# Kernel tuning notes

Hardware: AMD Instinct MI355X
Metric: run time of the kernel (lower is better)

## Reference

```python
import jax, jax.numpy as jnp
import numpy as np
import math

PS = 16            # patch size for SigmaPredictor
HID = 8            # hidden_dim
SCALE = HID ** -0.5
SIGMA_CAP = 6.0    # BoundedSoftplus threshold
EPS_S = 1e-6       # BoundedSoftplus eps


def setup_inputs() -> dict:
    key = jax.random.key(0)
    ks = jax.random.split(key, 10)
    B, C, H, W = 2, 1, 384, 384
    d_in = C * PS * PS  # 256
    r = lambda k_, sh: jax.random.normal(k_, sh, dtype=jnp.float32) * 0.1
    z = lambda sh: jnp.zeros(sh, dtype=jnp.float32)
    return {
        "x": jax.random.uniform(ks[0], (B, C, H, W), dtype=jnp.float32),
        "Wq": r(ks[1], (d_in, HID)), "bq": z((HID,)),
        "Wk": r(ks[2], (d_in, HID)), "bk": z((HID,)),
        "Wv": r(ks[3], (d_in, HID)), "bv": z((HID,)),
        "Wsq": r(ks[4], (HID, HID)), "bsq": z((HID,)),
        "Wsk": r(ks[5], (HID, HID)), "bsk": z((HID,)),
        "Wsv": r(ks[6], (HID, HID)), "bsv": z((HID,)),
        "ln_g": jnp.ones((HID,), jnp.float32), "ln_b": z((HID,)),
        "Wp": r(ks[7], (HID, 3)),
        # bias ~4 -> sigmas ~4 -> kernel size k=13 (production-scale support)
        "bp": jnp.full((3,), 4.0, dtype=jnp.float32),
    }


def _attn(q, k, v):
    a = jax.nn.softmax(jnp.einsum('bnd,bmd->bnm', q, k) * SCALE, axis=-1)
    return jnp.einsum('bnm,bmd->bnd', a, v)


def _predict_sigmas(x, Wq, bq, Wk, bk, Wv, bv, Wsq, bsq, Wsk, bsk, Wsv, bsv, ln_g, ln_b, Wp, bp):
    b, c, h, w = x.shape
    Hp, Wn = h // PS, w // PS
    # unfold into non-overlapping patches: [B, Hp*Wn, C*PS*PS]
    pat = x.reshape(b, c, Hp, PS, Wn, PS).transpose(0, 2, 4, 1, 3, 5).reshape(b, Hp * Wn, c * PS * PS)
    feats = _attn(pat @ Wq + bq, pat @ Wk + bk, pat @ Wv + bv)
    o = _attn(feats @ Wsq + bsq, feats @ Wsk + bsk, feats @ Wsv + bsv)
    mu = o.mean(-1, keepdims=True)
    var = ((o - mu) ** 2).mean(-1, keepdims=True)
    o = (o - mu) / jnp.sqrt(var + 1e-5) * ln_g + ln_b
    s = jnp.minimum(jax.nn.softplus(o @ Wp + bp), SIGMA_CAP) + EPS_S  # BoundedSoftplus
    s = s.reshape(b, Hp, Wn, 3)
    # nearest-neighbor upsample to full resolution: [B, H, W, 3]
    return jnp.repeat(jnp.repeat(s, PS, axis=1), PS, axis=2)


def _bilateral(x, s, k):
    b, c, h, w = x.shape
    sx, sy, sr = s[..., 0], s[..., 1], s[..., 2]
    half = k // 2
    xp = jnp.pad(x, ((0, 0), (0, 0), (half, half), (half, half)))
    # [B, C, H, W, k*k], dy-major to match torch unfold/meshgrid ordering
    patches = jnp.stack([xp[:, :, dy:dy + h, dx:dx + w]
                         for dy in range(k) for dx in range(k)], axis=-1)
    coords = jnp.arange(-half, half + 1, dtype=jnp.float32)
    yy, xx = jnp.meshgrid(coords, coords, indexing='ij')
    xx2 = (xx ** 2).reshape(-1)
    yy2 = (yy ** 2).reshape(-1)
    # spatial kernel [B, H, W, k*k]
    sp = jnp.exp(-xx2 / (2 * sx[..., None] ** 2) - yy2 / (2 * sy[..., None] ** 2))
    # range kernel (C == 1 branch) [B, C, H, W, k*k]
    rg = jnp.exp(-(x[..., None] - patches) ** 2 / (2 * sr[:, None, :, :, None] ** 2))
    comb = sp[:, None] * rg
    norm = comb / (comb.sum(-1, keepdims=True) + 1e-8)
    return (patches * norm).sum(-1)


def reference(x, Wq, bq, Wk, bk, Wv, bv, Wsq, bsq, Wsk, bsk, Wsv, bsv, ln_g, ln_b, Wp, bp):
    s = _predict_sigmas(x, Wq, bq, Wk, bk, Wv, bv, Wsq, bsq, Wsk, bsk, Wsv, bsv, ln_g, ln_b, Wp, bp)
    # data-dependent kernel size, computed eagerly (matches torch .item())
    m = float(jnp.maximum(s[..., 0].max(), s[..., 1].max()))
    k = int(2 * math.ceil(m + 1))
    if k % 2 == 0:
        k += 1
    return _bilateral(x, s, k)
```

## Files before the change

### kernel.cpp

```cpp
#include <hip/hip_runtime.h>

#define N_TOK 576
#define HP    24
#define PS    16
#define IMG   384
#define ATTN_SCALE 0.35355339059327373f

__global__ __launch_bounds__(256) void k_qkv1(
    const float* __restrict__ x,
    const float* __restrict__ Wq, const float* __restrict__ bq,
    const float* __restrict__ Wk, const float* __restrict__ bk,
    const float* __restrict__ Wv, const float* __restrict__ bv,
    float* __restrict__ q1, float* __restrict__ k1, float* __restrict__ v1,
    int* __restrict__ smax)
{
    const int lane = threadIdx.x & 63, wv = threadIdx.x >> 6;
    const int idx = blockIdx.x*4 + wv;
    const int b = idx / N_TOK, n = idx % N_TOK;
    const int py = n / HP, px = n % HP;

    if (idx == 0 && lane == 0) atomicExch(smax, 0);

    const int iy = lane >> 2, ix0 = (lane & 3) * 4;
    const float4 pv = *(const float4*)
        &x[b*IMG*IMG + (py*PS + iy)*IMG + px*PS + ix0];

    float acc[24];
#pragma unroll
    for (int j = 0; j < 24; ++j) acc[j] = 0.f;

#pragma unroll
    for (int j = 0; j < 4; ++j) {
        const int t = 4*lane + j;
        const float p = ((const float*)&pv)[j];
#pragma unroll
        for (int h = 0; h < 8; ++h) {
            acc[h]      += p * Wq[t*8 + h];
            acc[8 + h]  += p * Wk[t*8 + h];
            acc[16 + h] += p * Wv[t*8 + h];
        }
    }
#pragma unroll
    for (int off = 32; off; off >>= 1)
#pragma unroll
        for (int j = 0; j < 24; ++j) acc[j] += __shfl_xor(acc[j], off);

    if (lane == 0) {
#pragma unroll
        for (int h = 0; h < 8; ++h) {
            q1[idx*8 + h] = acc[h]      + bq[h];
            k1[idx*8 + h] = acc[8 + h]  + bk[h];
            v1[idx*8 + h] = acc[16 + h] + bv[h];
        }
    }
}

__global__ __launch_bounds__(256) void k_attn1(
    const float* __restrict__ q1, const float* __restrict__ k1, const float* __restrict__ v1,
    const float* __restrict__ Wsq, const float* __restrict__ bsq,
    const float* __restrict__ Wsk, const float* __restrict__ bsk,
    const float* __restrict__ Wsv, const float* __restrict__ bsv,
    float* __restrict__ q2, float* __restrict__ k2, float* __restrict__ v2)
{
    const int lane = threadIdx.x & 63;
    const int wv   = threadIdx.x >> 6;
    const int tok  = blockIdx.x*4 + wv;
    const int b    = tok / N_TOK;

    const float4 qa = *(const float4*)&q1[tok*8];
    const float4 qb = *(const float4*)&q1[tok*8 + 4];

    const float* kbp = k1 + b*N_TOK*8;
    const float* vbp = v1 + b*N_TOK*8;

    float sc[9], mx = -1e30f;
#pragma unroll
    for (int ch = 0; ch < 9; ++ch) {
        const float4* kp = (const float4*)(kbp + (ch*64 + lane)*8);
        const float4 k0 = kp[0], k1v = kp[1];
        float d = qa.x*k0.x + qa.y*k0.y + qa.z*k0.z + qa.w*k0.w
                + qb.x*k1v.x + qb.y*k1v.y + qb.z*k1v.z + qb.w*k1v.w;
        d *= ATTN_SCALE;
        sc[ch] = d;
        mx = fmaxf(mx, d);
    }
#pragma unroll
    for (int off = 32; off; off >>= 1) mx = fmaxf(mx, __shfl_xor(mx, off));

    float ssum = 0.f, o[8];
#pragma unroll
    for (int h = 0; h < 8; ++h) o[h] = 0.f;
#pragma unroll
    for (int ch = 0; ch < 9; ++ch) {
        const float p = __expf(sc[ch] - mx);
        ssum += p;
        const float4* vp = (const float4*)(vbp + (ch*64 + lane)*8);
        const float4 v0 = vp[0], v1v = vp[1];
        o[0] += p*v0.x; o[1] += p*v0.y; o[2] += p*v0.z; o[3] += p*v0.w;
        o[4] += p*v1v.x; o[5] += p*v1v.y; o[6] += p*v1v.z; o[7] += p*v1v.w;
    }
#pragma unroll
    for (int off = 32; off; off >>= 1) {
        ssum += __shfl_xor(ssum, off);
#pragma unroll
        for (int h = 0; h < 8; ++h) o[h] += __shfl_xor(o[h], off);
    }
    const float inv = 1.f/ssum;
    float f[8];
#pragma unroll
    for (int h = 0; h < 8; ++h) f[h] = o[h]*inv;

    if (lane < 24) {
        const int mat = lane >> 3, h = lane & 7;
        const float* Wm = (mat==0)?Wsq:(mat==1)?Wsk:Wsv;
        const float* bm = (mat==0)?bsq:(mat==1)?bsk:bsv;
        float s = bm[h];
#pragma unroll
        for (int j = 0; j < 8; ++j) s += f[j]*Wm[j*8 + h];
        float* dst = (mat==0)?q2:(mat==1)?k2:v2;
        dst[tok*8 + h] = s;
    }
}

__global__ __launch_bounds__(256) void k_attn2(
    const float* __restrict__ q2, const float* __restrict__ k2, const float* __restrict__ v2,
    const float* __restrict__ ln_g, const float* __restrict__ ln_b,
    const float* __restrict__ Wp,   const float* __restrict__ bp,
    float* __restrict__ sig, int* __restrict__ smax)
{
    const int lane = threadIdx.x & 63;
    const int wv   = threadIdx.x >> 6;
    const int tok  = blockIdx.x*4 + wv;
    const int b    = tok / N_TOK;

    const float4 qa = *(const float4*)&q2[tok*8];
    const float4 qb = *(const float4*)&q2[tok*8 + 4];

    const float* kbp = k2 + b*N_TOK*8;
    const float* vbp = v2 + b*N_TOK*8;

    float sc[9], mx = -1e30f;
#pragma unroll
    for (int ch = 0; ch < 9; ++ch) {
        const float4* kp = (const float4*)(kbp + (ch*64 + lane)*8);
        const float4 k0 = kp[0], k1v = kp[1];
        float d = qa.x*k0.x + qa.y*k0.y + qa.z*k0.z + qa.w*k0.w
                + qb.x*k1v.x + qb.y*k1v.y + qb.z*k1v.z + qb.w*k1v.w;
        d *= ATTN_SCALE;
        sc[ch] = d;
        mx = fmaxf(mx, d);
    }
#pragma unroll
    for (int off = 32; off; off >>= 1) mx = fmaxf(mx, __shfl_xor(mx, off));

    float ssum = 0.f, o[8];
#pragma unroll
    for (int h = 0; h < 8; ++h) o[h] = 0.f;
#pragma unroll
    for (int ch = 0; ch < 9; ++ch) {
        const float p = __expf(sc[ch] - mx);
        ssum += p;
        const float4* vp = (const float4*)(vbp + (ch*64 + lane)*8);
        const float4 v0 = vp[0], v1v = vp[1];
        o[0] += p*v0.x; o[1] += p*v0.y; o[2] += p*v0.z; o[3] += p*v0.w;
        o[4] += p*v1v.x; o[5] += p*v1v.y; o[6] += p*v1v.z; o[7] += p*v1v.w;
    }
#pragma unroll
    for (int off = 32; off; off >>= 1) {
        ssum += __shfl_xor(ssum, off);
#pragma unroll
        for (int h = 0; h < 8; ++h) o[h] += __shfl_xor(o[h], off);
    }

    if (lane == 0) {
        const float inv = 1.f/ssum;
        float f[8];
        float mu = 0.f;
#pragma unroll
        for (int h = 0; h < 8; ++h) { f[h] = o[h]*inv; mu += f[h]; }
        mu *= 0.125f;
        float var = 0.f;
#pragma unroll
        for (int h = 0; h < 8; ++h) { const float d = f[h]-mu; var += d*d; }
        var *= 0.125f;
        const float rinv = rsqrtf(var + 1e-5f);
        float on[8];
#pragma unroll
        for (int h = 0; h < 8; ++h)
            on[h] = (f[h]-mu)*rinv*ln_g[h] + ln_b[h];
        float sv[3];
#pragma unroll
        for (int c = 0; c < 3; ++c) {
            float z = bp[c];
#pragma unroll
            for (int j = 0; j < 8; ++j) z += on[j]*Wp[j*3 + c];
            const float sp = (z > 20.f) ? z : log1pf(__expf(z));
            sv[c] = fminf(sp, 6.0f) + 1e-6f;
            sig[tok*3 + c] = sv[c];
        }
        atomicMax(smax, __float_as_int(fmaxf(sv[0], sv[1])));
    }
}

__global__ __launch_bounds__(256) void k_bilat(
    const float* __restrict__ x, const float* __restrict__ sig,
    int* __restrict__ smax, float* __restrict__ out)
{
    __shared__ float tile[32*40];
    __shared__ float spt[17*17];
    __shared__ int   s_half;

    const int blk = blockIdx.x;
    const int b  = blk / N_TOK;
    const int n  = blk % N_TOK;
    const int py = n / HP, px = n % HP;
    const int tx = threadIdx.x & 15, ty = threadIdx.x >> 4;

    if (threadIdx.x == 0) {
        const float m = __int_as_float(atomicMax(smax, 0));
        int h = (int)ceilf(m + 1.0f);
        if (h < 1) h = 1;
        if (h > 8) h = 8;
        s_half = h;
    }
    __syncthreads();
    const int half = s_half;
    const int k = 2*half + 1;
    const int tilew = PS + 2*half;

    const float sx = sig[blk*3 + 0];
    const float sy = sig[blk*3 + 1];
    const float sr = sig[blk*3 + 2];

    const float* xb = x + b*IMG*IMG;
    for (int yy = ty; yy < tilew; yy += 16) {
        const int gy = py*PS + yy - half;
        for (int xx = tx; xx < tilew; xx += 16) {
            const int gx = px*PS + xx - half;
            float v = 0.f;
            if ((unsigned)gy < IMG && (unsigned)gx < IMG)
                v = xb[gy*IMG + gx];
            tile[yy*40 + xx] = v;
        }
    }
    {
        const float axc = -0.5f/(sx*sx);
        const float ayc = -0.5f/(sy*sy);
        for (int i = threadIdx.x; i < k*k; i += 256) {
            const int dy = i / k, dx = i - dy*k;
            const float fy = (float)(dy - half), fx = (float)(dx - half);
            spt[i] = __expf(ayc*fy*fy + axc*fx*fx);
        }
    }
    __syncthreads();

    const float c   = tile[(ty+half)*40 + (tx+half)];
    const float ar2 = -0.72134752044448170f/(sr*sr);

    float num = 0.f, den = 0.f;
    for (int dy = 0; dy < k; ++dy) {
        const float* row = &tile[(ty+dy)*40 + tx];
        const float* spr = &spt[dy*k];
        for (int dx = 0; dx < k; ++dx) {
            const float pix = row[dx];
            const float d   = c - pix;
            const float w   = spr[dx] * exp2f(ar2*d*d);
            den += w;
            num += w*pix;
        }
    }
    out[b*IMG*IMG + (py*PS + ty)*IMG + (px*PS + tx)] = num/(den + 1e-8f);
}

extern "C" void kernel_launch(void* const* d_in, const int* in_sizes, int n_in,
                              void* d_out, int out_size, void* d_ws, size_t ws_size,
                              hipStream_t stream)
{
    const float* x    = (const float*)d_in[0];
    const float* Wq   = (const float*)d_in[1];
    const float* bq   = (const float*)d_in[2];
    const float* Wk   = (const float*)d_in[3];
    const float* bk   = (const float*)d_in[4];
    const float* Wv   = (const float*)d_in[5];
    const float* bv   = (const float*)d_in[6];
    const float* Wsq  = (const float*)d_in[7];
    const float* bsq  = (const float*)d_in[8];
    const float* Wsk  = (const float*)d_in[9];
    const float* bsk  = (const float*)d_in[10];
    const float* Wsv  = (const float*)d_in[11];
    const float* bsv  = (const float*)d_in[12];
    const float* ln_g = (const float*)d_in[13];
    const float* ln_b = (const float*)d_in[14];
    const float* Wp   = (const float*)d_in[15];
    const float* bp   = (const float*)d_in[16];

    float* W  = (float*)d_ws;
    float* q1 = W;
    float* k1 = W +  9216;
    float* v1 = W + 18432;
    float* q2 = W + 27648;
    float* k2 = W + 36864;
    float* v2 = W + 46080;
    float* sg = W + 55296;
    int* smax = (int*)(W + 58752);

    k_qkv1<<<2*N_TOK/4, 256, 0, stream>>>(x, Wq, bq, Wk, bk, Wv, bv,
                                          q1, k1, v1, smax);
    k_attn1<<<2*N_TOK/4, 256, 0, stream>>>(q1, k1, v1, Wsq, bsq, Wsk, bsk,
                                           Wsv, bsv, q2, k2, v2);
    k_attn2<<<2*N_TOK/4, 256, 0, stream>>>(q2, k2, v2, ln_g, ln_b, Wp, bp,
                                           sg, smax);
    k_bilat<<<2*N_TOK, 256, 0, stream>>>(x, sg, smax, (float*)d_out);
}
```

Before: 149.6 us.

## Fuse all four stages into one persistent kernel with grid barriers

Replaces the four separate launches (QKV projection, two attention stages, bilateral filter) with one persistent kernel of 576 blocks that sync through atomic-counter grid barriers. Queries stay in registers between stages, and sigmas go through shared memory instead of global buffers. Each block now runs two bilateral patches back to back. This removes launch overhead and intermediate round-trips, but relies on all 576 blocks being co-resident. It also adds a memset and leaves half the waves idle during the attention phases.

```diff
diff --git a/kernel.cpp b/kernel.cpp
--- a/kernel.cpp
+++ b/kernel.cpp
@@ -5,271 +5,278 @@
 #define PS    16
 #define IMG   384
 #define ATTN_SCALE 0.35355339059327373f
-
-__global__ __launch_bounds__(256) void k_qkv1(
+#define NBLK  576
+
+__device__ __forceinline__ void gbar(unsigned* cnt, unsigned* flag)
+{
+    __syncthreads();
+    if (threadIdx.x == 0) {
+        __threadfence();
+        const unsigned old = __hip_atomic_fetch_add(
+            cnt, 1u, __ATOMIC_ACQ_REL, __HIP_MEMORY_SCOPE_AGENT);
+        if (old == NBLK - 1u) {
+            __hip_atomic_store(flag, 1u, __ATOMIC_RELEASE,
+                               __HIP_MEMORY_SCOPE_AGENT);
+        } else {
+            while (!__hip_atomic_load(flag, __ATOMIC_RELAXED,
+                                      __HIP_MEMORY_SCOPE_AGENT))
+                __builtin_amdgcn_s_sleep(4);
+        }
+        __threadfence();
+    }
+    __syncthreads();
+}
+
+__global__ __launch_bounds__(256, 3) void k_all(
     const float* __restrict__ x,
     const float* __restrict__ Wq, const float* __restrict__ bq,
     const float* __restrict__ Wk, const float* __restrict__ bk,
     const float* __restrict__ Wv, const float* __restrict__ bv,
-    float* __restrict__ q1, float* __restrict__ k1, float* __restrict__ v1,
-    int* __restrict__ smax)
-{
-    const int lane = threadIdx.x & 63, wv = threadIdx.x >> 6;
-    const int idx = blockIdx.x*4 + wv;
-    const int b = idx / N_TOK, n = idx % N_TOK;
-    const int py = n / HP, px = n % HP;
-
-    if (idx == 0 && lane == 0) atomicExch(smax, 0);
-
-    const int iy = lane >> 2, ix0 = (lane & 3) * 4;
-    const float4 pv = *(const float4*)
-        &x[b*IMG*IMG + (py*PS + iy)*IMG + px*PS + ix0];
-
-    float acc[24];
-#pragma unroll
-    for (int j = 0; j < 24; ++j) acc[j] = 0.f;
-
-#pragma unroll
-    for (int j = 0; j < 4; ++j) {
-        const int t = 4*lane + j;
-        const float p = ((const float*)&pv)[j];
-#pragma unroll
-        for (int h = 0; h < 8; ++h) {
-            acc[h]      += p * Wq[t*8 + h];
-            acc[8 + h]  += p * Wk[t*8 + h];
-            acc[16 + h] += p * Wv[t*8 + h];
-        }
-    }
-#pragma unroll
-    for (int off = 32; off; off >>= 1)
-#pragma unroll
-        for (int j = 0; j < 24; ++j) acc[j] += __shfl_xor(acc[j], off);
-
-    if (lane == 0) {
-#pragma unroll
-        for (int h = 0; h < 8; ++h) {
-            q1[idx*8 + h] = acc[h]      + bq[h];
-            k1[idx*8 + h] = acc[8 + h]  + bk[h];
-            v1[idx*8 + h] = acc[16 + h] + bv[h];
-        }
-    }
-}
-
-__global__ __launch_bounds__(256) void k_attn1(
-    const float* __restrict__ q1, const float* __restrict__ k1, const float* __restrict__ v1,
     const float* __restrict__ Wsq, const float* __restrict__ bsq,
     const float* __restrict__ Wsk, const float* __restrict__ bsk,
     const float* __restrict__ Wsv, const float* __restrict__ bsv,
-    float* __restrict__ q2, float* __restrict__ k2, float* __restrict__ v2)
-{
-    const int lane = threadIdx.x & 63;
-    const int wv   = threadIdx.x >> 6;
-    const int tok  = blockIdx.x*4 + wv;
-    const int b    = tok / N_TOK;
-
-    const float4 qa = *(const float4*)&q1[tok*8];
-    const float4 qb = *(const float4*)&q1[tok*8 + 4];
-
-    const float* kbp = k1 + b*N_TOK*8;
-    const float* vbp = v1 + b*N_TOK*8;
-
-    float sc[9], mx = -1e30f;
-#pragma unroll
-    for (int ch = 0; ch < 9; ++ch) {
-        const float4* kp = (const float4*)(kbp + (ch*64 + lane)*8);
-        const float4 k0 = kp[0], k1v = kp[1];
-        float d = qa.x*k0.x + qa.y*k0.y + qa.z*k0.z + qa.w*k0.w
-                + qb.x*k1v.x + qb.y*k1v.y + qb.z*k1v.z + qb.w*k1v.w;
-        d *= ATTN_SCALE;
-        sc[ch] = d;
-        mx = fmaxf(mx, d);
-    }
-#pragma unroll
-    for (int off = 32; off; off >>= 1) mx = fmaxf(mx, __shfl_xor(mx, off));
-
-    float ssum = 0.f, o[8];
-#pragma unroll
-    for (int h = 0; h < 8; ++h) o[h] = 0.f;
-#pragma unroll
-    for (int ch = 0; ch < 9; ++ch) {
-        const float p = __expf(sc[ch] - mx);
-        ssum += p;
-        const float4* vp = (const float4*)(vbp + (ch*64 + lane)*8);
-        const float4 v0 = vp[0], v1v = vp[1];
-        o[0] += p*v0.x; o[1] += p*v0.y; o[2] += p*v0.z; o[3] += p*v0.w;
-        o[4] += p*v1v.x; o[5] += p*v1v.y; o[6] += p*v1v.z; o[7] += p*v1v.w;
-    }
-#pragma unroll
-    for (int off = 32; off; off >>= 1) {
-        ssum += __shfl_xor(ssum, off);
-#pragma unroll
-        for (int h = 0; h < 8; ++h) o[h] += __shfl_xor(o[h], off);
-    }
-    const float inv = 1.f/ssum;
-    float f[8];
-#pragma unroll
-    for (int h = 0; h < 8; ++h) f[h] = o[h]*inv;
-
-    if (lane < 24) {
-        const int mat = lane >> 3, h = lane & 7;
-        const float* Wm = (mat==0)?Wsq:(mat==1)?Wsk:Wsv;
-        const float* bm = (mat==0)?bsq:(mat==1)?bsk:bsv;
-        float s = bm[h];
-#pragma unroll
-        for (int j = 0; j < 8; ++j) s += f[j]*Wm[j*8 + h];
-        float* dst = (mat==0)?q2:(mat==1)?k2:v2;
-        dst[tok*8 + h] = s;
-    }
-}
-
-__global__ __launch_bounds__(256) void k_attn2(
-    const float* __restrict__ q2, const float* __restrict__ k2, const float* __restrict__ v2,
     const float* __restrict__ ln_g, const float* __restrict__ ln_b,
     const float* __restrict__ Wp,   const float* __restrict__ bp,
-    float* __restrict__ sig, int* __restrict__ smax)
-{
-    const int lane = threadIdx.x & 63;
-    const int wv   = threadIdx.x >> 6;
-    const int tok  = blockIdx.x*4 + wv;
-    const int b    = tok / N_TOK;
-
-    const float4 qa = *(const float4*)&q2[tok*8];
-    const float4 qb = *(const float4*)&q2[tok*8 + 4];
-
-    const float* kbp = k2 + b*N_TOK*8;
-    const float* vbp = v2 + b*N_TOK*8;
-
-    float sc[9], mx = -1e30f;
-#pragma unroll
-    for (int ch = 0; ch < 9; ++ch) {
-        const float4* kp = (const float4*)(kbp + (ch*64 + lane)*8);
-        const float4 k0 = kp[0], k1v = kp[1];
-        float d = qa.x*k0.x + qa.y*k0.y + qa.z*k0.z + qa.w*k0.w
-                + qb.x*k1v.x + qb.y*k1v.y + qb.z*k1v.z + qb.w*k1v.w;
-        d *= ATTN_SCALE;
-        sc[ch] = d;
-        mx = fmaxf(mx, d);
-    }
-#pragma unroll
-    for (int off = 32; off; off >>= 1) mx = fmaxf(mx, __shfl_xor(mx, off));
-
-    float ssum = 0.f, o[8];
-#pragma unroll
-    for (int h = 0; h < 8; ++h) o[h] = 0.f;
-#pragma unroll
-    for (int ch = 0; ch < 9; ++ch) {
-        const float p = __expf(sc[ch] - mx);
-        ssum += p;
-        const float4* vp = (const float4*)(vbp + (ch*64 + lane)*8);
-        const float4 v0 = vp[0], v1v = vp[1];
-        o[0] += p*v0.x; o[1] += p*v0.y; o[2] += p*v0.z; o[3] += p*v0.w;
-        o[4] += p*v1v.x; o[5] += p*v1v.y; o[6] += p*v1v.z; o[7] += p*v1v.w;
-    }
-#pragma unroll
-    for (int off = 32; off; off >>= 1) {
-        ssum += __shfl_xor(ssum, off);
-#pragma unroll
-        for (int h = 0; h < 8; ++h) o[h] += __shfl_xor(o[h], off);
-    }
-
-    if (lane == 0) {
-        const float inv = 1.f/ssum;
-        float f[8];
-        float mu = 0.f;
-#pragma unroll
-        for (int h = 0; h < 8; ++h) { f[h] = o[h]*inv; mu += f[h]; }
-        mu *= 0.125f;
-        float var = 0.f;
-#pragma unroll
-        for (int h = 0; h < 8; ++h) { const float d = f[h]-mu; var += d*d; }
-        var *= 0.125f;
-        const float rinv = rsqrtf(var + 1e-5f);
-        float on[8];
-#pragma unroll
-        for (int h = 0; h < 8; ++h)
-            on[h] = (f[h]-mu)*rinv*ln_g[h] + ln_b[h];
-        float sv[3];
-#pragma unroll
-        for (int c = 0; c < 3; ++c) {
-            float z = bp[c];
-#pragma unroll
-            for (int j = 0; j < 8; ++j) z += on[j]*Wp[j*3 + c];
-            const float sp = (z > 20.f) ? z : log1pf(__expf(z));
-            sv[c] = fminf(sp, 6.0f) + 1e-6f;
-            sig[tok*3 + c] = sv[c];
-        }
-        atomicMax(smax, __float_as_int(fmaxf(sv[0], sv[1])));
-    }
-}
-
-__global__ __launch_bounds__(256) void k_bilat(
-    const float* __restrict__ x, const float* __restrict__ sig,
-    int* __restrict__ smax, float* __restrict__ out)
+    float* __restrict__ k1, float* __restrict__ v1,
+    float* __restrict__ k2, float* __restrict__ v2,
+    unsigned* __restrict__ ctl,
+    float* __restrict__ out)
 {
     __shared__ float tile[32*40];
     __shared__ float spt[17*17];
+    __shared__ float s_sig[2][3];
     __shared__ int   s_half;
 
+    const int t = threadIdx.x, lane = t & 63, w = t >> 6;
     const int blk = blockIdx.x;
-    const int b  = blk / N_TOK;
-    const int n  = blk % N_TOK;
-    const int py = n / HP, px = n % HP;
-    const int tx = threadIdx.x & 15, ty = threadIdx.x >> 4;
-
-    if (threadIdx.x == 0) {
-        const float m = __int_as_float(atomicMax(smax, 0));
+
+    float qv[8];
+    if (w < 2) {
+        const int p  = blk*2 + w;
+        const int b  = p / N_TOK, n = p % N_TOK;
+        const int py = n / HP, px = n % HP;
+        const int iy = lane >> 2, ix0 = (lane & 3) * 4;
+        const float4 pv = *(const float4*)
+            &x[b*IMG*IMG + (py*PS + iy)*IMG + px*PS + ix0];
+
+        float acc[24];
+#pragma unroll
+        for (int j = 0; j < 24; ++j) acc[j] = 0.f;
+#pragma unroll
+        for (int j = 0; j < 4; ++j) {
+            const int ft = 4*lane + j;
+            const float pvj = ((const float*)&pv)[j];
+#pragma unroll
+            for (int h = 0; h < 8; ++h) {
+                acc[h]      += pvj * Wq[ft*8 + h];
+                acc[8 + h]  += pvj * Wk[ft*8 + h];
+                acc[16 + h] += pvj * Wv[ft*8 + h];
+            }
+        }
+#pragma unroll
+        for (int off = 32; off; off >>= 1)
+#pragma unroll
+            for (int j = 0; j < 24; ++j) acc[j] += __shfl_xor(acc[j], off);
+
+#pragma unroll
+        for (int h = 0; h < 8; ++h) qv[h] = acc[h] + bq[h];
+        if (lane >= 8 && lane < 16)
+            k1[p*8 + (lane & 7)] = acc[8 + (lane & 7)]  + bk[lane & 7];
+        if (lane >= 16 && lane < 24)
+            v1[p*8 + (lane & 7)] = acc[16 + (lane & 7)] + bv[lane & 7];
+    }
+    gbar(ctl + 0, ctl + 1);
+
+    float qv2[8];
+    if (w < 2) {
+        const int tok = blk*2 + w;
+        const int b   = tok / N_TOK;
+        const float* kbp = k1 + b*N_TOK*8;
+        const float* vbp = v1 + b*N_TOK*8;
+
+        float sc[9], mx = -1e30f;
+#pragma unroll
+        for (int ch = 0; ch < 9; ++ch) {
+            const float4* kp = (const float4*)(kbp + (ch*64 + lane)*8);
+            const float4 k0 = kp[0], k1r = kp[1];
+            float d = qv[0]*k0.x + qv[1]*k0.y + qv[2]*k0.z + qv[3]*k0.w
+                    + qv[4]*k1r.x + qv[5]*k1r.y + qv[6]*k1r.z + qv[7]*k1r.w;
+            sc[ch] = d * ATTN_SCALE;
+            mx = fmaxf(mx, sc[ch]);
+        }
+#pragma unroll
+        for (int off = 32; off; off >>= 1) mx = fmaxf(mx, __shfl_xor(mx, off));
+
+        float ssum = 0.f, o[8];
+#pragma unroll
+        for (int h = 0; h < 8; ++h) o[h] = 0.f;
+#pragma unroll
+        for (int ch = 0; ch < 9; ++ch) {
+            const float pw = __expf(sc[ch] - mx);
+            ssum += pw;
+            const float4* vp = (const float4*)(vbp + (ch*64 + lane)*8);
+            const float4 v0 = vp[0], v1r = vp[1];
+            o[0] += pw*v0.x; o[1] += pw*v0.y; o[2] += pw*v0.z; o[3] += pw*v0.w;
+            o[4] += pw*v1r.x; o[5] += pw*v1r.y; o[6] += pw*v1r.z; o[7] += pw*v1r.w;
+        }
+#pragma unroll
+        for (int off = 32; off; off >>= 1) {
+            ssum += __shfl_xor(ssum, off);
+#pragma unroll
+            for (int h = 0; h < 8; ++h) o[h] += __shfl_xor(o[h], off);
+        }
+        const float inv = 1.f/ssum;
+        float f[8];
+#pragma unroll
+        for (int h = 0; h < 8; ++h) f[h] = o[h]*inv;
+
+        float sproj = 0.f;
+        if (lane < 24) {
+            const int mat = lane >> 3, h = lane & 7;
+            const float* Wm = (mat==0)?Wsq:(mat==1)?Wsk:Wsv;
+            const float* bm = (mat==0)?bsq:(mat==1)?bsk:bsv;
+            float s = bm[h];
+#pragma unroll
+            for (int j = 0; j < 8; ++j) s += f[j]*Wm[j*8 + h];
+            sproj = s;
+            if (mat == 1) k2[tok*8 + h] = s;
+            if (mat == 2) v2[tok*8 + h] = s;
+        }
+#pragma unroll
+        for (int h = 0; h < 8; ++h) qv2[h] = __shfl(sproj, h);
+    }
+    gbar(ctl + 2, ctl + 3);
+
+    if (w < 2) {
+        const int tok = blk*2 + w;
+        const int b   = tok / N_TOK;
+        const float* kbp = k2 + b*N_TOK*8;
+        const float* vbp = v2 + b*N_TOK*8;
+
+        float sc[9], mx = -1e30f;
+#pragma unroll
+        for (int ch = 0; ch < 9; ++ch) {
+            const float4* kp = (const float4*)(kbp + (ch*64 + lane)*8);
+            const float4 k0 = kp[0], k1r = kp[1];
+            float d = qv2[0]*k0.x + qv2[1]*k0.y + qv2[2]*k0.z + qv2[3]*k0.w
+                    + qv2[4]*k1r.x + qv2[5]*k1r.y + qv2[6]*k1r.z + qv2[7]*k1r.w;
+            sc[ch] = d * ATTN_SCALE;
+            mx = fmaxf(mx, sc[ch]);
+        }
+#pragma unroll
+        for (int off = 32; off; off >>= 1) mx = fmaxf(mx, __shfl_xor(mx, off));
+
+        float ssum = 0.f, o[8];
+#pragma unroll
+        for (int h = 0; h < 8; ++h) o[h] = 0.f;
+#pragma unroll
+        for (int ch = 0; ch < 9; ++ch) {
+            const float pw = __expf(sc[ch] - mx);
+            ssum += pw;
+            const float4* vp = (const float4*)(vbp + (ch*64 + lane)*8);
+            const float4 v0 = vp[0], v1r = vp[1];
+            o[0] += pw*v0.x; o[1] += pw*v0.y; o[2] += pw*v0.z; o[3] += pw*v0.w;
+            o[4] += pw*v1r.x; o[5] += pw*v1r.y; o[6] += pw*v1r.z; o[7] += pw*v1r.w;
+        }
+#pragma unroll
+        for (int off = 32; off; off >>= 1) {
+            ssum += __shfl_xor(ssum, off);
+#pragma unroll
+            for (int h = 0; h < 8; ++h) o[h] += __shfl_xor(o[h], off);
+        }
+
+        if (lane == 0) {
+            const float inv = 1.f/ssum;
+            float f[8];
+            float mu = 0.f;
+#pragma unroll
+            for (int h = 0; h < 8; ++h) { f[h] = o[h]*inv; mu += f[h]; }
+            mu *= 0.125f;
+            float var = 0.f;
+#pragma unroll
+            for (int h = 0; h < 8; ++h) { const float d = f[h]-mu; var += d*d; }
+            var *= 0.125f;
+            const float rinv = rsqrtf(var + 1e-5f);
+            float on[8];
+#pragma unroll
+            for (int h = 0; h < 8; ++h)
+                on[h] = (f[h]-mu)*rinv*ln_g[h] + ln_b[h];
+            float sv[3];
+#pragma unroll
+            for (int c = 0; c < 3; ++c) {
+                float z = bp[c];
+#pragma unroll
+                for (int j = 0; j < 8; ++j) z += on[j]*Wp[j*3 + c];
+                const float sp = (z > 20.f) ? z : log1pf(__expf(z));
+                sv[c] = fminf(sp, 6.0f) + 1e-6f;
+                s_sig[w][c] = sv[c];
+            }
+            atomicMax((int*)(ctl + 6), __float_as_int(fmaxf(sv[0], sv[1])));
+        }
+    }
+    gbar(ctl + 4, ctl + 5);
+
+    if (t == 0) {
+        const int mi = __hip_atomic_load((const int*)(ctl + 6),
+                                         __ATOMIC_RELAXED,
+                                         __HIP_MEMORY_SCOPE_AGENT);
+        const float m = __int_as_float(mi);
         int h = (int)ceilf(m + 1.0f);
         if (h < 1) h = 1;
         if (h > 8) h = 8;
         s_half = h;
     }
     __syncthreads();
-    const int half = s_half;
-    const int k = 2*half + 1;
+    const int half  = s_half;
+    const int k     = 2*half + 1;
     const int tilew = PS + 2*half;
-
-    const float sx = sig[blk*3 + 0];
-    const float sy = sig[blk*3 + 1];
-    const float sr = sig[blk*3 + 2];
-
-    const float* xb = x + b*IMG*IMG;
-    for (int yy = ty; yy < tilew; yy += 16) {
-        const int gy = py*PS + yy - half;
-        for (int xx = tx; xx < tilew; xx += 16) {
-            const int gx = px*PS + xx - half;
-            float v = 0.f;
-            if ((unsigned)gy < IMG && (unsigned)gx < IMG)
-                v = xb[gy*IMG + gx];
-            tile[yy*40 + xx] = v;
-        }
-    }
-    {
-        const float axc = -0.5f/(sx*sx);
-        const float ayc = -0.5f/(sy*sy);
-        for (int i = threadIdx.x; i < k*k; i += 256) {
-            const int dy = i / k, dx = i - dy*k;
-            const float fy = (float)(dy - half), fx = (float)(dx - half);
-            spt[i] = __expf(ayc*fy*fy + axc*fx*fx);
-        }
-    }
-    __syncthreads();
-
-    const float c   = tile[(ty+half)*40 + (tx+half)];
-    const float ar2 = -0.72134752044448170f/(sr*sr);
-
-    float num = 0.f, den = 0.f;
-    for (int dy = 0; dy < k; ++dy) {
-        const float* row = &tile[(ty+dy)*40 + tx];
-        const float* spr = &spt[dy*k];
-        for (int dx = 0; dx < k; ++dx) {
-            const float pix = row[dx];
-            const float d   = c - pix;
-            const float w   = spr[dx] * exp2f(ar2*d*d);
-            den += w;
-            num += w*pix;
-        }
-    }
-    out[b*IMG*IMG + (py*PS + ty)*IMG + (px*PS + tx)] = num/(den + 1e-8f);
+    const int tx = t & 15, ty = t >> 4;
+
+    for (int i = 0; i < 2; ++i) {
+        const int p  = blk*2 + i;
+        const int b  = p / N_TOK, n = p % N_TOK;
+        const int py = n / HP, px = n % HP;
+        const float sx = s_sig[i][0], sy = s_sig[i][1], sr = s_sig[i][2];
+        const float* xb = x + b*IMG*IMG;
+
+        for (int yy = ty; yy < tilew; yy += 16) {
+            const int gy = py*PS + yy - half;
+            for (int xx = tx; xx < tilew; xx += 16) {
+                const int gx = px*PS + xx - half;
+                float v = 0.f;
+                if ((unsigned)gy < IMG && (unsigned)gx < IMG)
+                    v = xb[gy*IMG + gx];
+                tile[yy*40 + xx] = v;
+            }
+        }
+        {
+            const float axc = -0.5f/(sx*sx);
+            const float ayc = -0.5f/(sy*sy);
+            for (int ii = t; ii < k*k; ii += 256) {
+                const int dy = ii / k, dx = ii - dy*k;
+                const float fy = (float)(dy - half), fx = (float)(dx - half);
+                spt[ii] = __expf(ayc*fy*fy + axc*fx*fx);
+            }
+        }
+        __syncthreads();
+
+        const float c   = tile[(ty+half)*40 + (tx+half)];
+        const float ar2 = -0.72134752044448170f/(sr*sr);
+        float num = 0.f, den = 0.f;
+        for (int dy = 0; dy < k; ++dy) {
+            const float* row = &tile[(ty+dy)*40 + tx];
+            const float* spr = &spt[dy*k];
+            for (int dx = 0; dx < k; ++dx) {
+                const float pix = row[dx];
+                const float d   = c - pix;
+                const float wgt = spr[dx] * exp2f(ar2*d*d);
+                den += wgt;
+                num += wgt*pix;
+            }
+        }
+        out[b*IMG*IMG + (py*PS + ty)*IMG + (px*PS + tx)] = num/(den + 1e-8f);
+        __syncthreads();
+    }
 }
 
 extern "C" void kernel_launch(void* const* d_in, const int* in_sizes, int n_in,
@@ -295,20 +302,16 @@
     const float* bp   = (const float*)d_in[16];
 
     float* W  = (float*)d_ws;
-    float* q1 = W;
-    float* k1 = W +  9216;
-    float* v1 = W + 18432;
-    float* q2 = W + 27648;
-    float* k2 = W + 36864;
-    float* v2 = W + 46080;
-    float* sg = W + 55296;
-    int* smax = (int*)(W + 58752);
-
-    k_qkv1<<<2*N_TOK/4, 256, 0, stream>>>(x, Wq, bq, Wk, bk, Wv, bv,
-                                          q1, k1, v1, smax);
-    k_attn1<<<2*N_TOK/4, 256, 0, stream>>>(q1, k1, v1, Wsq, bsq, Wsk, bsk,
-                                           Wsv, bsv, q2, k2, v2);
-    k_attn2<<<2*N_TOK/4, 256, 0, stream>>>(q2, k2, v2, ln_g, ln_b, Wp, bp,
-                                           sg, smax);
-    k_bilat<<<2*N_TOK, 256, 0, stream>>>(x, sg, smax, (float*)d_out);
+    float* k1 = W;
+    float* v1 = W +  9216;
+    float* k2 = W + 18432;
+    float* v2 = W + 27648;
+    unsigned* ctl = (unsigned*)(W + 36864);
+
+    hipMemsetAsync(ctl, 0, 32, stream);
+
+    k_all<<<NBLK, 256, 0, stream>>>(x, Wq, bq, Wk, bk, Wv, bv,
+                                    Wsq, bsq, Wsk, bsk, Wsv, bsv,
+                                    ln_g, ln_b, Wp, bp,
+                                    k1, v1, k2, v2, ctl, (float*)d_out);
 }
```

Measured after the change: 267.1 us. 78.5% more time.
